# Optimization experiments

Measured on AMD Instinct MI355X. Metric: run time of the kernel, lower is better.

The kernel has to match this reference:

```python
import jax, jax.numpy as jnp
import numpy as np

# Model config (mirrors Mamba2Block(dim=256) with mamba_ssm defaults)
D_MODEL = 256
EXPAND = 2
D_INNER = D_MODEL * EXPAND          # 512
HEADDIM = D_MODEL * EXPAND // 8     # 64
NHEADS = D_INNER // HEADDIM         # 8
D_STATE = 64
D_CONV = 4
CONV_DIM = D_INNER + 2 * D_STATE    # 640 (ngroups=1)
D_IN_PROJ = 2 * D_INNER + 2 * D_STATE + NHEADS  # 1160
BATCH, SEQLEN = 2, 2048
EPS = 1e-5


def setup_inputs() -> dict:
    key = jax.random.key(0)
    ks = jax.random.split(key, 12)
    s = 0.02
    return {
        "hidden_states": jax.random.normal(ks[0], (BATCH, SEQLEN, D_MODEL), jnp.float32),
        "norm_w": jnp.ones((D_MODEL,), jnp.float32),
        "norm_b": jnp.zeros((D_MODEL,), jnp.float32),
        "W_in": jax.random.normal(ks[1], (D_MODEL, D_IN_PROJ), jnp.float32) * s,
        "conv_w": jax.random.normal(ks[2], (CONV_DIM, D_CONV), jnp.float32) * 0.25,
        "conv_b": jnp.zeros((CONV_DIM,), jnp.float32),
        "dt_bias": jax.random.uniform(ks[3], (NHEADS,), jnp.float32),
        "A_log": jax.random.uniform(ks[4], (NHEADS,), jnp.float32),  # A = -exp(A_log) in (-e, -1]
        "D_param": jnp.ones((NHEADS,), jnp.float32),
        "rms_w": jnp.ones((D_INNER,), jnp.float32),
        "W_out": jax.random.normal(ks[5], (D_INNER, D_MODEL), jnp.float32) * s,
    }


def _layer_norm(x, w, b):
    mu = jnp.mean(x, -1, keepdims=True)
    var = jnp.mean((x - mu) ** 2, -1, keepdims=True)
    return (x - mu) * jax.lax.rsqrt(var + EPS) * w + b


def _causal_depthwise_conv(x, w, b):
    # x: [B,L,C], w: [C,K] depthwise causal conv
    B, L, C = x.shape
    K = w.shape[1]
    xp = jnp.pad(x, ((0, 0), (K - 1, 0), (0, 0)))
    y = b
    for k in range(K):  # K=4, fixed small kernel
        y = y + w[:, k] * xp[:, k:k + L, :]
    return y


def reference(hidden_states, norm_w, norm_b, W_in, conv_w, conv_b, dt_bias, A_log, D_param, rms_w, W_out):
    B, L, D = hidden_states.shape
    residual = hidden_states                       # residual is None, drop_path=0
    x = _layer_norm(residual, norm_w, norm_b)      # pre-norm

    zxbcdt = jnp.einsum("bld,de->ble", x, W_in)    # [B,L,2*Di+2*N+H]
    z = zxbcdt[..., :D_INNER]
    xBC = zxbcdt[..., D_INNER:D_INNER + CONV_DIM]
    dt = zxbcdt[..., -NHEADS:]

    xBC = jax.nn.silu(_causal_depthwise_conv(xBC, conv_w, conv_b))
    xs = xBC[..., :D_INNER]
    Bm = xBC[..., D_INNER:D_INNER + D_STATE]       # [B,L,N] (ngroups=1)
    Cm = xBC[..., D_INNER + D_STATE:]              # [B,L,N]

    dt = jax.nn.softplus(dt + dt_bias)             # [B,L,H]
    A = -jnp.exp(A_log)                            # [H]
    dA = jnp.exp(dt * A)                           # [B,L,H]

    xh = xs.reshape(B, L, NHEADS, HEADDIM)         # [B,L,H,P]
    dtx = dt[..., None] * xh                       # [B,L,H,P]

    def step(s, inp):
        dA_t, dtx_t, B_t, C_t = inp                # [B,H],[B,H,P],[B,N],[B,N]
        s = s * dA_t[:, :, None, None] + dtx_t[..., None] * B_t[:, None, None, :]
        y_t = jnp.einsum("bhpn,bn->bhp", s, C_t)
        return s, y_t

    s0 = jnp.zeros((B, NHEADS, HEADDIM, D_STATE), hidden_states.dtype)
    xs_in = (jnp.swapaxes(dA, 0, 1), jnp.swapaxes(dtx, 0, 1),
             jnp.swapaxes(Bm, 0, 1), jnp.swapaxes(Cm, 0, 1))
    _, ys = jax.lax.scan(step, s0, xs_in)          # ys: [L,B,H,P]
    y = jnp.swapaxes(ys, 0, 1) + D_param[None, None, :, None] * xh  # skip term
    y = y.reshape(B, L, D_INNER)

    # gated RMSNorm (norm_before_gate=False): rmsnorm(y * silu(z)) * rms_w
    g = y * jax.nn.silu(z)
    g = g * jax.lax.rsqrt(jnp.mean(g * g, -1, keepdims=True) + EPS) * rms_w

    out = jnp.einsum("bld,de->ble", g, W_out)
    return out, residual
```

## Files before the change

### kernel.cpp

```cpp
#include <hip/hip_runtime.h>
#include <hip/hip_bf16.h>

#define BATCH 2
#define SEQLEN 2048
#define DMODEL 256
#define DINNER 512
#define NHEADS 8
#define HEADDIM 64
#define DSTATE 64
#define CONVDIM 640
#define DINPROJ 1160
#define NTOK (BATCH*SEQLEN)
#define Q 64
#define NCH (SEQLEN/Q)
#define NPAD_IN 1216
#define TS 72
#define RS3 196

typedef short v8s __attribute__((ext_vector_type(8)));
typedef float v4f __attribute__((ext_vector_type(4)));

__device__ __forceinline__ unsigned short f2bf(float f){
    __hip_bfloat16 h = __float2bfloat16(f);
    return *reinterpret_cast<unsigned short*>(&h);
}
__device__ __forceinline__ float bf2f(unsigned short u){
    unsigned int x = ((unsigned int)u) << 16;
    return __uint_as_float(x);
}

__global__ __launch_bounds__(256) void k_prep(
        const float* __restrict__ hid, const float* __restrict__ nw, const float* __restrict__ nb,
        const float* __restrict__ Win, const float* __restrict__ Wout,
        float* __restrict__ res, unsigned short* __restrict__ Xb,
        unsigned short* __restrict__ Wti, unsigned short* __restrict__ Wto){
    int bx = blockIdx.x;
    int t = threadIdx.x;
    if(bx < 256){
        __shared__ float xs[16][DMODEL];
        int tok0 = bx*16;
        for(int i=0;i<16;i++){
            int idx = i*256+t; int j = idx>>8, c = idx&255;
            float v = hid[(size_t)(tok0+j)*DMODEL + c];
            xs[j][c] = v;
            res[(size_t)(tok0+j)*DMODEL + c] = v;
        }
        __syncthreads();
        int g = t>>4, il = t&15;
        float sum=0.f, sumsq=0.f;
        for(int i=0;i<16;i++){ float v = xs[g][il*16+i]; sum += v; sumsq += v*v; }
        #pragma unroll
        for(int m=1;m<16;m<<=1){ sum += __shfl_xor(sum,m); sumsq += __shfl_xor(sumsq,m); }
        float mu   = sum*(1.f/256.f);
        float var  = sumsq*(1.f/256.f) - mu*mu;
        float rstd = rsqrtf(var + 1e-5f);
        for(int i=0;i<16;i++){
            int c = il*16+i;
            xs[g][c] = (xs[g][c]-mu)*rstd*nw[c] + nb[c];
        }
        __syncthreads();
        for(int i=0;i<16;i++){
            int idx = i*256+t; int j = idx>>8, c = idx&255;
            Xb[(size_t)(tok0+j)*DMODEL + c] = f2bf(xs[j][c]);
        }
    } else if(bx < 256 + NPAD_IN/4){
        int n0 = (bx-256)*4, k = t;
        #pragma unroll
        for(int i=0;i<4;i++){
            int n = n0+i;
            float v = (n < DINPROJ) ? Win[(size_t)k*DINPROJ + n] : 0.f;
            Wti[(size_t)n*DMODEL + k] = f2bf(v);
        }
    } else {
        int n0 = (bx - 256 - NPAD_IN/4)*4;
        #pragma unroll
        for(int kk=0;kk<2;kk++){
            int k = t + kk*256;
            #pragma unroll
            for(int i=0;i<4;i++){
                int n = n0+i;
                Wto[(size_t)n*DINNER + k] = f2bf(Wout[(size_t)k*DMODEL + n]);
            }
        }
    }
}

template<int BF16OUT>
__global__ __launch_bounds__(256) void k_gemm(
        const unsigned short* __restrict__ A, const unsigned short* __restrict__ Bt,
        float* __restrict__ Cf, unsigned short* __restrict__ Cb, int K, int Ncols){
    __shared__ __align__(16) unsigned short As[128*40];
    __shared__ __align__(16) unsigned short Bs[64*40];
    int t = threadIdx.x;
    int lane = t & 63, w = t >> 6;
    int lanelow = lane & 15, quad = lane >> 4;
    int tok0 = blockIdx.x * 128;
    int n0   = blockIdx.y * 64;
    v4f acc[2][4];
    #pragma unroll
    for(int mi=0;mi<2;mi++)
        #pragma unroll
        for(int ni=0;ni<4;ni++)
            acc[mi][ni] = (v4f){0.f,0.f,0.f,0.f};
    for(int k0=0; k0<K; k0+=32){
        __syncthreads();
        #pragma unroll
        for(int cc=0; cc<2; cc++){
            int c = t + cc*256;
            int row = c>>2, off = c&3;
            uint4 v = *(const uint4*)(A + (size_t)(tok0+row)*K + k0 + off*8);
            *(uint4*)&As[row*40 + off*8] = v;
        }
        {
            int row = t>>2, off = t&3;
            uint4 v = *(const uint4*)(Bt + (size_t)(n0+row)*K + k0 + off*8);
            *(uint4*)&Bs[row*40 + off*8] = v;
        }
        __syncthreads();
        v8s a0 = *(const v8s*)&As[(w*32 +      lanelow)*40 + quad*8];
        v8s a1 = *(const v8s*)&As[(w*32 + 16 + lanelow)*40 + quad*8];
        v8s b[4];
        #pragma unroll
        for(int ni=0;ni<4;ni++)
            b[ni] = *(const v8s*)&Bs[(ni*16 + lanelow)*40 + quad*8];
        #pragma unroll
        for(int ni=0;ni<4;ni++){
            acc[0][ni] = __builtin_amdgcn_mfma_f32_16x16x32_bf16(a0, b[ni], acc[0][ni], 0,0,0);
            acc[1][ni] = __builtin_amdgcn_mfma_f32_16x16x32_bf16(a1, b[ni], acc[1][ni], 0,0,0);
        }
    }
    #pragma unroll
    for(int mi=0;mi<2;mi++){
        #pragma unroll
        for(int ni=0;ni<4;ni++){
            int col = n0 + ni*16 + lanelow;
            if(col < Ncols){
                #pragma unroll
                for(int r=0;r<4;r++){
                    int row = tok0 + w*32 + mi*16 + quad*4 + r;
                    if(BF16OUT) Cb[(size_t)row*Ncols + col] = f2bf(acc[mi][ni][r]);
                    else        Cf[(size_t)row*Ncols + col] = acc[mi][ni][r];
                }
            }
        }
    }
}

__global__ __launch_bounds__(256) void k_chunk1(
        const unsigned short* __restrict__ zxb, const float* __restrict__ conv_w, const float* __restrict__ conv_b,
        const float* __restrict__ dt_bias, const float* __restrict__ A_log, const float* __restrict__ D_param,
        unsigned short* __restrict__ yw16, unsigned short* __restrict__ contrib16,
        float* __restrict__ Larr, float* __restrict__ decayArr, unsigned short* __restrict__ Ccv){
    int blk = blockIdx.x;
    int c = blk & 31, h = (blk>>5)&7, b = blk>>8;
    int t = threadIdx.x;
    int lane = t & 63, w = t >> 6;
    int lanelow = lane & 15, quad = lane >> 4;
    __shared__ __align__(16) unsigned short Cb[64*TS];
    __shared__ __align__(16) unsigned short Bb[64*TS];
    __shared__ __align__(16) unsigned short BtW[64*TS];
    __shared__ __align__(16) unsigned short Xt[64*TS];
    __shared__ __align__(16) unsigned short Gbuf[64*TS];
    __shared__ __align__(16) unsigned short raw[19*RS3];
    __shared__ float Ls[Q], dts[Q], wch[Q];
    int l0 = c*Q;
    int bh = b*NHEADS + h;
    const unsigned short* zbase = zxb + (size_t)(b*SEQLEN + l0)*DINPROJ;
    if(t < Q){
        float v = bf2f(zbase[(size_t)t*DINPROJ + (DINPROJ-NHEADS) + h]) + dt_bias[h];
        float dt = (v > 20.f) ? v : log1pf(__expf(v));
        float A  = -__expf(A_log[h]);
        float ld = dt*A;
        #pragma unroll
        for(int off=1; off<64; off<<=1){
            float u = __shfl_up(ld, off);
            if(lane >= off) ld += u;
        }
        Ls[t] = ld; dts[t] = dt;
    }
    __syncthreads();
    float L63 = Ls[Q-1];
    if(t < Q) wch[t] = __expf(L63 - Ls[t]) * dts[t];
    unsigned short* CcP = Ccv + ((size_t)b*NCH + c)*4096;
    for(int s=0; s<4; s++){
        __syncthreads();
        #pragma unroll
        for(int i=0;i<4;i++){
            int u = t + 256*i;
            if(u < 19*48){
                int row = u/48, seg = u%48;
                int l = l0 + s*16 - 3 + row;
                int gcol = (seg<16) ? (DINNER + h*HEADDIM + seg*4) : (2*DINNER + (seg-16)*4);
                ushort4 v;
                if(l >= 0) v = *(const ushort4*)(zxb + ((size_t)b*SEQLEN + l)*DINPROJ + gcol);
                else { v.x=0; v.y=0; v.z=0; v.w=0; }
                *(ushort4*)&raw[row*RS3 + seg*4] = v;
            }
        }
        __syncthreads();
        #pragma unroll
        for(int i=0;i<3;i++){
            int u = t + 256*i;
            int stl = u & 15, grp = u >> 4;
            int st = s*16 + stl;
            int ch = grp*4;
            float xk[4][4];
            #pragma unroll
            for(int k=0;k<4;k++){
                ushort4 v = *(const ushort4*)&raw[(stl+k)*RS3 + ch];
                xk[k][0]=bf2f(v.x); xk[k][1]=bf2f(v.y); xk[k][2]=bf2f(v.z); xk[k][3]=bf2f(v.w);
            }
            float wst = wch[st];
            #pragma unroll
            for(int j=0;j<4;j++){
                int chj = ch+j;
                int cc = (chj<64) ? (h*HEADDIM + chj) : (448 + chj);
                float4 wv = *(const float4*)&conv_w[cc*4];
                float acc = conv_b[cc] + wv.x*xk[0][j] + wv.y*xk[1][j] + wv.z*xk[2][j] + wv.w*xk[3][j];
                float sv = acc/(1.f+__expf(-acc));
                if(chj < 64){
                    Xt[chj*TS + st] = f2bf(sv);
                } else if(chj < 128){
                    int n = chj-64;
                    Bb[st*TS + n]  = f2bf(sv);
                    BtW[n*TS + st] = f2bf(sv*wst);
                } else {
                    int n = chj-128;
                    unsigned short sb16 = f2bf(sv);
                    Cb[st*TS + n] = sb16;
                    if(h==0) CcP[st*64 + n] = sb16;
                }
            }
        }
    }
    __syncthreads();
    v4f g[4];
    #pragma unroll
    for(int nt=0;nt<4;nt++) g[nt] = (v4f){0.f,0.f,0.f,0.f};
    #pragma unroll
    for(int kk=0;kk<2;kk++){
        v8s a = *(const v8s*)&Cb[(w*16+lanelow)*TS + kk*32 + quad*8];
        #pragma unroll
        for(int nt=0;nt<4;nt++){
            v8s bb = *(const v8s*)&Bb[(nt*16+lanelow)*TS + kk*32 + quad*8];
            g[nt] = __builtin_amdgcn_mfma_f32_16x16x32_bf16(a, bb, g[nt], 0,0,0);
        }
    }
    float Lrow[4];
    #pragma unroll
    for(int r=0;r<4;r++) Lrow[r] = Ls[w*16 + quad*4 + r];
    #pragma unroll
    for(int nt=0;nt<4;nt++){
        int col = nt*16 + lanelow;
        float Lc = Ls[col], dtc = dts[col];
        #pragma unroll
        for(int r=0;r<4;r++){
            int rowg = w*16 + quad*4 + r;
            float val = (col <= rowg) ? g[nt][r] * __expf(Lrow[r]-Lc) * dtc : 0.f;
            Gbuf[rowg*TS + col] = f2bf(val);
        }
    }
    __syncthreads();
    v4f ya[4], sa[4];
    #pragma unroll
    for(int nt=0;nt<4;nt++){ ya[nt]=(v4f){0.f,0.f,0.f,0.f}; sa[nt]=(v4f){0.f,0.f,0.f,0.f}; }
    #pragma unroll
    for(int kk=0;kk<2;kk++){
        v8s ag = *(const v8s*)&Gbuf[(w*16+lanelow)*TS + kk*32 + quad*8];
        v8s ax = *(const v8s*)&Xt[(w*16+lanelow)*TS + kk*32 + quad*8];
        #pragma unroll
        for(int nt=0;nt<4;nt++){
            v8s bx = *(const v8s*)&Xt[(nt*16+lanelow)*TS + kk*32 + quad*8];
            v8s bw = *(const v8s*)&BtW[(nt*16+lanelow)*TS + kk*32 + quad*8];
            ya[nt] = __builtin_amdgcn_mfma_f32_16x16x32_bf16(ag, bx, ya[nt], 0,0,0);
            sa[nt] = __builtin_amdgcn_mfma_f32_16x16x32_bf16(ax, bw, sa[nt], 0,0,0);
        }
    }
    float Dp = D_param[h];
    #pragma unroll
    for(int nt=0;nt<4;nt++){
        int col = nt*16 + lanelow;
        #pragma unroll
        for(int r=0;r<4;r++){
            int i = w*16 + quad*4 + r;
            float xval = bf2f(Xt[col*TS + i]);
            yw16[((size_t)b*SEQLEN + l0 + i)*DINNER + h*HEADDIM + col] = f2bf(ya[nt][r] + Dp*xval);
            contrib16[(((size_t)bh*NCH + c)*64 + i)*64 + col] = f2bf(sa[nt][r]);
        }
    }
    if(t < Q) Larr[((size_t)bh*NCH + c)*Q + t] = Ls[t];
    if(t == 0) decayArr[bh*NCH + c] = __expf(L63);
}

__global__ __launch_bounds__(256) void k_chunk2(const unsigned short* __restrict__ contrib16,
                                                const float* __restrict__ decayArr,
                                                unsigned short* __restrict__ Sb){
    int bh = blockIdx.x >> 4;
    int part = blockIdx.x & 15;
    int e = part*256 + threadIdx.x;
    const size_t base = (size_t)bh*NCH*4096 + e;
    float vals[NCH];
    #pragma unroll
    for(int c=0;c<NCH;c++) vals[c] = bf2f(contrib16[base + (size_t)c*4096]);
    float s = 0.f;
    #pragma unroll
    for(int c=0;c<NCH;c++){
        Sb[base + (size_t)c*4096] = f2bf(s);
        s = fmaf(s, decayArr[bh*NCH + c], vals[c]);
    }
}

__global__ __launch_bounds__(512) void k_tail(
        const unsigned short* __restrict__ Ccv, const unsigned short* __restrict__ Sb,
        const float* __restrict__ Larr, const unsigned short* __restrict__ yw16,
        const unsigned short* __restrict__ zxb, const float* __restrict__ rms_w,
        unsigned short* __restrict__ Gb){
    int blk = blockIdx.x;
    int half = blk & 1, c = (blk>>1) & 31, b = blk >> 6;
    int t = threadIdx.x;
    int h = t >> 6, lane = t & 63;
    int lanelow = lane & 15, quad = lane >> 4;
    int bh = b*NHEADS + h;
    __shared__ float wsum[8][32];
    __shared__ float rstdS[32];
    const unsigned short* Cp = Ccv + ((size_t)b*NCH + c)*4096;
    const unsigned short* Sp = Sb + ((size_t)bh*NCH + c)*4096;
    v8s a[2][2];
    #pragma unroll
    for(int rt=0;rt<2;rt++){
        int row = half*32 + rt*16 + lanelow;
        a[rt][0] = *(const v8s*)(Cp + row*64 + quad*8);
        a[rt][1] = *(const v8s*)(Cp + row*64 + 32 + quad*8);
    }
    v8s s[4][2];
    #pragma unroll
    for(int nt=0;nt<4;nt++){
        s[nt][0] = *(const v8s*)(Sp + (nt*16+lanelow)*64 + quad*8);
        s[nt][1] = *(const v8s*)(Sp + (nt*16+lanelow)*64 + 32 + quad*8);
    }
    float g[2][4][4];
    float sq[2][4];
    const float* Lp = Larr + ((size_t)bh*NCH + c)*Q;
    #pragma unroll
    for(int rt=0;rt<2;rt++){
        float eL[4];
        #pragma unroll
        for(int r=0;r<4;r++) eL[r] = __expf(Lp[half*32 + rt*16 + quad*4 + r]);
        #pragma unroll
        for(int nt=0;nt<4;nt++){
            v4f acc = (v4f){0.f,0.f,0.f,0.f};
            acc = __builtin_amdgcn_mfma_f32_16x16x32_bf16(a[rt][0], s[nt][0], acc, 0,0,0);
            acc = __builtin_amdgcn_mfma_f32_16x16x32_bf16(a[rt][1], s[nt][1], acc, 0,0,0);
            int col = h*HEADDIM + nt*16 + lanelow;
            #pragma unroll
            for(int r=0;r<4;r++){
                int i = half*32 + rt*16 + quad*4 + r;
                size_t tok = (size_t)b*SEQLEN + c*Q + i;
                float yv = acc[r]*eL[r] + bf2f(yw16[tok*DINNER + col]);
                float z  = bf2f(zxb[tok*DINPROJ + col]);
                float gg = yv * (z/(1.f+__expf(-z)));
                g[rt][nt][r] = gg;
                sq[rt][r] = (nt==0 ? gg*gg : sq[rt][r] + gg*gg);
            }
        }
    }
    #pragma unroll
    for(int rt=0;rt<2;rt++)
        #pragma unroll
        for(int r=0;r<4;r++){
            float v = sq[rt][r];
            #pragma unroll
            for(int m=1;m<16;m<<=1) v += __shfl_xor(v, m);
            sq[rt][r] = v;
        }
    if(lanelow==0){
        #pragma unroll
        for(int rt=0;rt<2;rt++)
            #pragma unroll
            for(int r=0;r<4;r++)
                wsum[h][rt*16 + quad*4 + r] = sq[rt][r];
    }
    __syncthreads();
    if(t < 32){
        float tot = 0.f;
        #pragma unroll
        for(int hh=0;hh<8;hh++) tot += wsum[hh][t];
        rstdS[t] = rsqrtf(tot*(1.f/512.f) + 1e-5f);
    }
    __syncthreads();
    #pragma unroll
    for(int rt=0;rt<2;rt++){
        #pragma unroll
        for(int nt=0;nt<4;nt++){
            int col = h*HEADDIM + nt*16 + lanelow;
            float rw = rms_w[col];
            #pragma unroll
            for(int r=0;r<4;r++){
                int i = rt*16 + quad*4 + r;
                Gb[((size_t)b*SEQLEN + c*Q + half*32 + i)*DINNER + col] = f2bf(g[rt][nt][r] * rstdS[i] * rw);
            }
        }
    }
}

extern "C" void kernel_launch(void* const* d_in, const int* in_sizes, int n_in,
                              void* d_out, int out_size, void* d_ws, size_t ws_size,
                              hipStream_t stream) {
    const float* hid     = (const float*)d_in[0];
    const float* norm_w  = (const float*)d_in[1];
    const float* norm_b  = (const float*)d_in[2];
    const float* Win     = (const float*)d_in[3];
    const float* conv_w  = (const float*)d_in[4];
    const float* conv_b  = (const float*)d_in[5];
    const float* dt_bias = (const float*)d_in[6];
    const float* A_log   = (const float*)d_in[7];
    const float* D_param = (const float*)d_in[8];
    const float* rms_w   = (const float*)d_in[9];
    const float* Wout    = (const float*)d_in[10];

    unsigned short* contrib16 = (unsigned short*)d_ws;
    float* Larr    = (float*)(contrib16 + (size_t)16*NCH*4096);
    float* decayA  = Larr + (size_t)16*NCH*Q;
    unsigned short* zxb  = (unsigned short*)(decayA + 512);
    unsigned short* yw16 = zxb + (size_t)NTOK*DINPROJ;
    unsigned short* Sb   = yw16 + (size_t)NTOK*DINNER;
    unsigned short* Ccv  = Sb + (size_t)16*NCH*4096;
    unsigned short* Xb   = Ccv + (size_t)BATCH*NCH*4096;
    unsigned short* Gb   = Xb + (size_t)NTOK*DMODEL;
    unsigned short* Wti  = Gb + (size_t)NTOK*DINNER;
    unsigned short* Wto  = Wti + (size_t)NPAD_IN*DMODEL;

    float* out = (float*)d_out;
    float* res = out + (size_t)NTOK*DMODEL;

    k_prep<<<256 + NPAD_IN/4 + DMODEL/4, 256, 0, stream>>>(hid, norm_w, norm_b, Win, Wout, res, Xb, Wti, Wto);
    k_gemm<1><<<dim3(NTOK/128, NPAD_IN/64), 256, 0, stream>>>(Xb, Wti, nullptr, zxb, DMODEL, DINPROJ);
    k_chunk1<<<BATCH*NHEADS*NCH, 256, 0, stream>>>(zxb, conv_w, conv_b, dt_bias, A_log, D_param,
                                                   yw16, contrib16, Larr, decayA, Ccv);
    k_chunk2<<<256, 256, 0, stream>>>(contrib16, decayA, Sb);
    k_tail<<<BATCH*NCH*2, 512, 0, stream>>>(Ccv, Sb, Larr, yw16, zxb, rms_w, Gb);
    k_gemm<0><<<dim3(NTOK/128, DMODEL/64), 256, 0, stream>>>(Gb, Wto, out, nullptr, DINNER, DMODEL);
}
```

Measured before the change: 138.8 us.

## Retile input/output projection GEMMs and split tail kernel into quarter chunks

The input projection GEMM now uses 128x128 tiles, with each wave computing a 64x64 sub-tile, and the weight padding grows to 1280 columns. The output projection gets its own kernel with smaller 64x64 tiles so more blocks are launched. The tail kernel splits each chunk into four 16-row blocks instead of two 32-row halves, doubling its grid. Together these aim at better MFMA reuse in the large GEMM and more parallelism in the small GEMM and the tail. The cost is extra padded compute, and the LDS tiles drop the row padding so bank conflicts may increase.

```diff
diff --git a/kernel.cpp b/kernel.cpp
--- a/kernel.cpp
+++ b/kernel.cpp
@@ -13,7 +13,7 @@
 #define NTOK (BATCH*SEQLEN)
 #define Q 64
 #define NCH (SEQLEN/Q)
-#define NPAD_IN 1216
+#define NPAD2 1280
 #define TS 72
 #define RS3 196
 
@@ -63,7 +63,7 @@
             int idx = i*256+t; int j = idx>>8, c = idx&255;
             Xb[(size_t)(tok0+j)*DMODEL + c] = f2bf(xs[j][c]);
         }
-    } else if(bx < 256 + NPAD_IN/4){
+    } else if(bx < 256 + NPAD2/4){
         int n0 = (bx-256)*4, k = t;
         #pragma unroll
         for(int i=0;i<4;i++){
@@ -72,7 +72,7 @@
             Wti[(size_t)n*DMODEL + k] = f2bf(v);
         }
     } else {
-        int n0 = (bx - 256 - NPAD_IN/4)*4;
+        int n0 = (bx - 256 - NPAD2/4)*4;
         #pragma unroll
         for(int kk=0;kk<2;kk++){
             int k = t + kk*256;
@@ -85,63 +85,95 @@
     }
 }
 
-template<int BF16OUT>
-__global__ __launch_bounds__(256) void k_gemm(
+__global__ __launch_bounds__(256) void k_gemm_in(
         const unsigned short* __restrict__ A, const unsigned short* __restrict__ Bt,
-        float* __restrict__ Cf, unsigned short* __restrict__ Cb, int K, int Ncols){
-    __shared__ __align__(16) unsigned short As[128*40];
-    __shared__ __align__(16) unsigned short Bs[64*40];
+        unsigned short* __restrict__ zxb){
+    __shared__ __align__(16) unsigned short As[128*32];
+    __shared__ __align__(16) unsigned short Bs[128*32];
     int t = threadIdx.x;
     int lane = t & 63, w = t >> 6;
     int lanelow = lane & 15, quad = lane >> 4;
     int tok0 = blockIdx.x * 128;
-    int n0   = blockIdx.y * 64;
-    v4f acc[2][4];
-    #pragma unroll
-    for(int mi=0;mi<2;mi++)
+    int n0   = blockIdx.y * 128;
+    int rw = (w & 1) * 64, cw = (w >> 1) * 64;
+    v4f acc[4][4];
+    #pragma unroll
+    for(int mi=0;mi<4;mi++)
         #pragma unroll
         for(int ni=0;ni<4;ni++)
             acc[mi][ni] = (v4f){0.f,0.f,0.f,0.f};
-    for(int k0=0; k0<K; k0+=32){
+    for(int k0=0; k0<DMODEL; k0+=32){
         __syncthreads();
         #pragma unroll
         for(int cc=0; cc<2; cc++){
-            int c = t + cc*256;
-            int row = c>>2, off = c&3;
-            uint4 v = *(const uint4*)(A + (size_t)(tok0+row)*K + k0 + off*8);
-            *(uint4*)&As[row*40 + off*8] = v;
-        }
+            int u = t + cc*256;
+            int row = u>>2, off = u&3;
+            *(uint4*)&As[row*32 + off*8] = *(const uint4*)(A + (size_t)(tok0+row)*DMODEL + k0 + off*8);
+            *(uint4*)&Bs[row*32 + off*8] = *(const uint4*)(Bt + (size_t)(n0+row)*DMODEL + k0 + off*8);
+        }
+        __syncthreads();
+        v8s a[4], b[4];
+        #pragma unroll
+        for(int mi=0;mi<4;mi++) a[mi] = *(const v8s*)&As[(rw + mi*16 + lanelow)*32 + quad*8];
+        #pragma unroll
+        for(int ni=0;ni<4;ni++) b[ni] = *(const v8s*)&Bs[(cw + ni*16 + lanelow)*32 + quad*8];
+        #pragma unroll
+        for(int mi=0;mi<4;mi++)
+            #pragma unroll
+            for(int ni=0;ni<4;ni++)
+                acc[mi][ni] = __builtin_amdgcn_mfma_f32_16x16x32_bf16(a[mi], b[ni], acc[mi][ni], 0,0,0);
+    }
+    #pragma unroll
+    for(int mi=0;mi<4;mi++){
+        #pragma unroll
+        for(int ni=0;ni<4;ni++){
+            int col = n0 + cw + ni*16 + lanelow;
+            if(col < DINPROJ){
+                #pragma unroll
+                for(int r=0;r<4;r++){
+                    int row = tok0 + rw + mi*16 + quad*4 + r;
+                    zxb[(size_t)row*DINPROJ + col] = f2bf(acc[mi][ni][r]);
+                }
+            }
+        }
+    }
+}
+
+__global__ __launch_bounds__(256) void k_gemm_out(
+        const unsigned short* __restrict__ Gb, const unsigned short* __restrict__ Wto,
+        float* __restrict__ out){
+    __shared__ __align__(16) unsigned short As[64*32];
+    __shared__ __align__(16) unsigned short Bs[64*32];
+    int t = threadIdx.x;
+    int lane = t & 63, w = t >> 6;
+    int lanelow = lane & 15, quad = lane >> 4;
+    int tok0 = blockIdx.x * 64;
+    int n0   = blockIdx.y * 64;
+    v4f acc[4];
+    #pragma unroll
+    for(int ni=0;ni<4;ni++) acc[ni] = (v4f){0.f,0.f,0.f,0.f};
+    for(int k0=0; k0<DINNER; k0+=32){
+        __syncthreads();
         {
             int row = t>>2, off = t&3;
-            uint4 v = *(const uint4*)(Bt + (size_t)(n0+row)*K + k0 + off*8);
-            *(uint4*)&Bs[row*40 + off*8] = v;
-        }
-        __syncthreads();
-        v8s a0 = *(const v8s*)&As[(w*32 +      lanelow)*40 + quad*8];
-        v8s a1 = *(const v8s*)&As[(w*32 + 16 + lanelow)*40 + quad*8];
-        v8s b[4];
-        #pragma unroll
-        for(int ni=0;ni<4;ni++)
-            b[ni] = *(const v8s*)&Bs[(ni*16 + lanelow)*40 + quad*8];
+            *(uint4*)&As[row*32 + off*8] = *(const uint4*)(Gb + (size_t)(tok0+row)*DINNER + k0 + off*8);
+            *(uint4*)&Bs[row*32 + off*8] = *(const uint4*)(Wto + (size_t)(n0+row)*DINNER + k0 + off*8);
+        }
+        __syncthreads();
+        v8s a = *(const v8s*)&As[(w*16 + lanelow)*32 + quad*8];
         #pragma unroll
         for(int ni=0;ni<4;ni++){
-            acc[0][ni] = __builtin_amdgcn_mfma_f32_16x16x32_bf16(a0, b[ni], acc[0][ni], 0,0,0);
-            acc[1][ni] = __builtin_amdgcn_mfma_f32_16x16x32_bf16(a1, b[ni], acc[1][ni], 0,0,0);
-        }
-    }
-    #pragma unroll
-    for(int mi=0;mi<2;mi++){
-        #pragma unroll
-        for(int ni=0;ni<4;ni++){
-            int col = n0 + ni*16 + lanelow;
-            if(col < Ncols){
-                #pragma unroll
-                for(int r=0;r<4;r++){
-                    int row = tok0 + w*32 + mi*16 + quad*4 + r;
-                    if(BF16OUT) Cb[(size_t)row*Ncols + col] = f2bf(acc[mi][ni][r]);
-                    else        Cf[(size_t)row*Ncols + col] = acc[mi][ni][r];
-                }
-            }
+            v8s b = *(const v8s*)&Bs[(ni*16 + lanelow)*32 + quad*8];
+            acc[ni] = __builtin_amdgcn_mfma_f32_16x16x32_bf16(a, b, acc[ni], 0,0,0);
+        }
+    }
+    #pragma unroll
+    for(int ni=0;ni<4;ni++){
+        int col = n0 + ni*16 + lanelow;
+        #pragma unroll
+        for(int r=0;r<4;r++){
+            int row = tok0 + w*16 + quad*4 + r;
+            out[(size_t)row*DMODEL + col] = acc[ni][r];
         }
     }
 }
@@ -316,72 +348,60 @@
         const unsigned short* __restrict__ zxb, const float* __restrict__ rms_w,
         unsigned short* __restrict__ Gb){
     int blk = blockIdx.x;
-    int half = blk & 1, c = (blk>>1) & 31, b = blk >> 6;
+    int q4 = blk & 3, c = (blk>>2) & 31, b = blk >> 7;
     int t = threadIdx.x;
     int h = t >> 6, lane = t & 63;
     int lanelow = lane & 15, quad = lane >> 4;
     int bh = b*NHEADS + h;
-    __shared__ float wsum[8][32];
-    __shared__ float rstdS[32];
+    __shared__ float wsum[8][16];
+    __shared__ float rstdS[16];
     const unsigned short* Cp = Ccv + ((size_t)b*NCH + c)*4096;
     const unsigned short* Sp = Sb + ((size_t)bh*NCH + c)*4096;
-    v8s a[2][2];
-    #pragma unroll
-    for(int rt=0;rt<2;rt++){
-        int row = half*32 + rt*16 + lanelow;
-        a[rt][0] = *(const v8s*)(Cp + row*64 + quad*8);
-        a[rt][1] = *(const v8s*)(Cp + row*64 + 32 + quad*8);
-    }
+    int row0 = q4*16;
+    v8s a0 = *(const v8s*)(Cp + (row0+lanelow)*64 + quad*8);
+    v8s a1 = *(const v8s*)(Cp + (row0+lanelow)*64 + 32 + quad*8);
     v8s s[4][2];
     #pragma unroll
     for(int nt=0;nt<4;nt++){
         s[nt][0] = *(const v8s*)(Sp + (nt*16+lanelow)*64 + quad*8);
         s[nt][1] = *(const v8s*)(Sp + (nt*16+lanelow)*64 + 32 + quad*8);
     }
-    float g[2][4][4];
-    float sq[2][4];
+    float g[4][4];
+    float sq[4] = {0.f,0.f,0.f,0.f};
     const float* Lp = Larr + ((size_t)bh*NCH + c)*Q;
-    #pragma unroll
-    for(int rt=0;rt<2;rt++){
-        float eL[4];
-        #pragma unroll
-        for(int r=0;r<4;r++) eL[r] = __expf(Lp[half*32 + rt*16 + quad*4 + r]);
-        #pragma unroll
-        for(int nt=0;nt<4;nt++){
-            v4f acc = (v4f){0.f,0.f,0.f,0.f};
-            acc = __builtin_amdgcn_mfma_f32_16x16x32_bf16(a[rt][0], s[nt][0], acc, 0,0,0);
-            acc = __builtin_amdgcn_mfma_f32_16x16x32_bf16(a[rt][1], s[nt][1], acc, 0,0,0);
-            int col = h*HEADDIM + nt*16 + lanelow;
-            #pragma unroll
-            for(int r=0;r<4;r++){
-                int i = half*32 + rt*16 + quad*4 + r;
-                size_t tok = (size_t)b*SEQLEN + c*Q + i;
-                float yv = acc[r]*eL[r] + bf2f(yw16[tok*DINNER + col]);
-                float z  = bf2f(zxb[tok*DINPROJ + col]);
-                float gg = yv * (z/(1.f+__expf(-z)));
-                g[rt][nt][r] = gg;
-                sq[rt][r] = (nt==0 ? gg*gg : sq[rt][r] + gg*gg);
-            }
-        }
-    }
-    #pragma unroll
-    for(int rt=0;rt<2;rt++)
+    float eL[4];
+    #pragma unroll
+    for(int r=0;r<4;r++) eL[r] = __expf(Lp[row0 + quad*4 + r]);
+    #pragma unroll
+    for(int nt=0;nt<4;nt++){
+        v4f acc = (v4f){0.f,0.f,0.f,0.f};
+        acc = __builtin_amdgcn_mfma_f32_16x16x32_bf16(a0, s[nt][0], acc, 0,0,0);
+        acc = __builtin_amdgcn_mfma_f32_16x16x32_bf16(a1, s[nt][1], acc, 0,0,0);
+        int col = h*HEADDIM + nt*16 + lanelow;
         #pragma unroll
         for(int r=0;r<4;r++){
-            float v = sq[rt][r];
-            #pragma unroll
-            for(int m=1;m<16;m<<=1) v += __shfl_xor(v, m);
-            sq[rt][r] = v;
-        }
+            int i = row0 + quad*4 + r;
+            size_t tok = (size_t)b*SEQLEN + c*Q + i;
+            float yv = acc[r]*eL[r] + bf2f(yw16[tok*DINNER + col]);
+            float z  = bf2f(zxb[tok*DINPROJ + col]);
+            float gg = yv * (z/(1.f+__expf(-z)));
+            g[nt][r] = gg;
+            sq[r] += gg*gg;
+        }
+    }
+    #pragma unroll
+    for(int r=0;r<4;r++){
+        float v = sq[r];
+        #pragma unroll
+        for(int m=1;m<16;m<<=1) v += __shfl_xor(v, m);
+        sq[r] = v;
+    }
     if(lanelow==0){
         #pragma unroll
-        for(int rt=0;rt<2;rt++)
-            #pragma unroll
-            for(int r=0;r<4;r++)
-                wsum[h][rt*16 + quad*4 + r] = sq[rt][r];
+        for(int r=0;r<4;r++) wsum[h][quad*4 + r] = sq[r];
     }
     __syncthreads();
-    if(t < 32){
+    if(t < 16){
         float tot = 0.f;
         #pragma unroll
         for(int hh=0;hh<8;hh++) tot += wsum[hh][t];
@@ -389,16 +409,13 @@
     }
     __syncthreads();
     #pragma unroll
-    for(int rt=0;rt<2;rt++){
-        #pragma unroll
-        for(int nt=0;nt<4;nt++){
-            int col = h*HEADDIM + nt*16 + lanelow;
-            float rw = rms_w[col];
-            #pragma unroll
-            for(int r=0;r<4;r++){
-                int i = rt*16 + quad*4 + r;
-                Gb[((size_t)b*SEQLEN + c*Q + half*32 + i)*DINNER + col] = f2bf(g[rt][nt][r] * rstdS[i] * rw);
-            }
+    for(int nt=0;nt<4;nt++){
+        int col = h*HEADDIM + nt*16 + lanelow;
+        float rw = rms_w[col];
+        #pragma unroll
+        for(int r=0;r<4;r++){
+            int i = row0 + quad*4 + r;
+            Gb[((size_t)b*SEQLEN + c*Q + i)*DINNER + col] = f2bf(g[nt][r] * rstdS[quad*4 + r] * rw);
         }
     }
 }
@@ -428,16 +445,16 @@
     unsigned short* Xb   = Ccv + (size_t)BATCH*NCH*4096;
     unsigned short* Gb   = Xb + (size_t)NTOK*DMODEL;
     unsigned short* Wti  = Gb + (size_t)NTOK*DINNER;
-    unsigned short* Wto  = Wti + (size_t)NPAD_IN*DMODEL;
+    unsigned short* Wto  = Wti + (size_t)NPAD2*DMODEL;
 
     float* out = (float*)d_out;
     float* res = out + (size_t)NTOK*DMODEL;
 
-    k_prep<<<256 + NPAD_IN/4 + DMODEL/4, 256, 0, stream>>>(hid, norm_w, norm_b, Win, Wout, res, Xb, Wti, Wto);
-    k_gemm<1><<<dim3(NTOK/128, NPAD_IN/64), 256, 0, stream>>>(Xb, Wti, nullptr, zxb, DMODEL, DINPROJ);
+    k_prep<<<256 + NPAD2/4 + DMODEL/4, 256, 0, stream>>>(hid, norm_w, norm_b, Win, Wout, res, Xb, Wti, Wto);
+    k_gemm_in<<<dim3(NTOK/128, NPAD2/128), 256, 0, stream>>>(Xb, Wti, zxb);
     k_chunk1<<<BATCH*NHEADS*NCH, 256, 0, stream>>>(zxb, conv_w, conv_b, dt_bias, A_log, D_param,
                                                    yw16, contrib16, Larr, decayA, Ccv);
     k_chunk2<<<256, 256, 0, stream>>>(contrib16, decayA, Sb);
-    k_tail<<<BATCH*NCH*2, 512, 0, stream>>>(Ccv, Sb, Larr, yw16, zxb, rms_w, Gb);
-    k_gemm<0><<<dim3(NTOK/128, DMODEL/64), 256, 0, stream>>>(Gb, Wto, out, nullptr, DINNER, DMODEL);
-}
+    k_tail<<<BATCH*NCH*4, 512, 0, stream>>>(Ccv, Sb, Larr, yw16, zxb, rms_w, Gb);
+    k_gemm_out<<<dim3(NTOK/64, DMODEL/64), 256, 0, stream>>>(Gb, Wto, out);
+}
```

Measured after the change: 129.4 us. 1.07x faster.
